# Optimization experiments

Hardware: AMD Instinct MI355X
Metric: run time of the kernel (lower is better)

Reference implementation:

```python
import jax, jax.numpy as jnp
import numpy as np

BS, T, N, E = 4, 6, 400, 3000
D = 100        # object_dim == state_dim == out_fts (forced by code)
NS = 30        # num states
NOBJ = 300     # object vocab
NET = 10       # n edge types
NSTEPS = 3     # GatedGraphConv n_steps


def setup_inputs() -> dict:
    key = jax.random.key(0)
    ks = jax.random.split(key, 16)
    def nrm(k, shape, s=0.05):
        return jax.random.normal(k, shape, jnp.float32) * s
    return dict(
        class_names=jax.random.randint(ks[0], (BS, T, N), 0, NOBJ),
        states=jax.random.uniform(ks[1], (BS, T, N, NS), jnp.float32),
        edges=jax.random.randint(ks[2], (BS, T, E, 2), 0, N),
        edge_types=jax.random.randint(ks[3], (BS, T, E), 0, NET),
        visibility=jax.random.uniform(ks[4], (BS, T, N), jnp.float32),
        mask_edges=jnp.ones((BS, T, E), jnp.float32),
        obj_emb=nrm(ks[5], (NOBJ, D)),
        state_W=nrm(ks[6], (D, NS)), state_b=jnp.zeros((D,), jnp.float32),
        c1_W=nrm(ks[7], (D, 2 * D)), c1_b=jnp.zeros((D,), jnp.float32),
        c2_W=nrm(ks[8], (D, D)), c2_b=jnp.zeros((D,), jnp.float32),
        edge_embed=nrm(ks[9], (NET, D * D)),
        g_wih=nrm(ks[10], (3 * D, D)), g_whh=nrm(ks[11], (3 * D, D)),
        g_bih=jnp.zeros((3 * D,), jnp.float32), g_bhh=jnp.zeros((3 * D,), jnp.float32),
        o_wih=nrm(ks[12], (3 * D, D)), o_whh=nrm(ks[13], (3 * D, D)),
    )


def _gru(x, h, wih, whh, bih=None, bhh=None):
    # torch.nn.GRUCell semantics
    gi = x @ wih.T
    gh = h @ whh.T
    if bih is not None:
        gi = gi + bih
        gh = gh + bhh
    ir, iz, inn = jnp.split(gi, 3, axis=-1)
    hr, hz, hn = jnp.split(gh, 3, axis=-1)
    r = jax.nn.sigmoid(ir + hr)
    z = jax.nn.sigmoid(iz + hz)
    n = jnp.tanh(inn + r * hn)
    return (1.0 - z) * n + z * h


def reference(class_names, states, edges, edge_types, visibility, mask_edges,
              obj_emb, state_W, state_b, c1_W, c1_b, c2_W, c2_b,
              edge_embed, g_wih, g_whh, g_bih, g_bhh, o_wih, o_whh):
    bs, t_len, n = class_names.shape
    # initial node representation (ClassNameStateRepresentation)
    emb = obj_emb[class_names]                       # [bs,T,N,D]
    st = states @ state_W.T + state_b                # [bs,T,N,D]
    x = jnp.concatenate([emb, st], -1)
    x = jax.nn.relu(x @ c1_W.T + c1_b) @ c2_W.T + c2_b  # [bs,T,N,D]

    off = (jnp.arange(bs) * n)[:, None]              # flatten batch into node axis
    h = jnp.zeros((bs * n, D), x.dtype)              # outer temporal GRU state
    reprs = []
    for t in range(t_len):
        h = _gru(x[:, t].reshape(bs * n, D), h, o_wih, o_whh)  # bias=False
        feat_flat = h                                 # [bs*N, D]
        src = (edges[:, t, :, 0] + off).reshape(-1)   # [bs*E]
        dst = (edges[:, t, :, 1] + off).reshape(-1)
        # per-edge DxD matrices, masked (as in original)
        W = edge_embed[edge_types[:, t].reshape(-1)].reshape(-1, D, D)
        W = W * mask_edges[:, t].reshape(-1)[:, None, None]
        # NOTE: original never updates feat_flat inside the n_steps loop,
        # so every step reads the same source features; we replicate that.
        feat_out = feat_flat
        for _ in range(NSTEPS):
            msg = jnp.einsum('eij,ej->ei', W, feat_flat[src])           # per-edge matvec
            a = jax.ops.segment_sum(msg, dst, num_segments=bs * n)     # scatter-add
            feat_out = _gru(a, feat_flat, g_wih, g_whh, g_bih, g_bhh)
        reprs.append(feat_out.reshape(bs, n, D) * visibility[:, t, :, None])
    node_reprs = jnp.stack(reprs, 1)                  # [bs,T,N,D]
    num_nodes = visibility.sum(-1) + 1e-9             # [bs,T]
    global_repr = (node_reprs * visibility[..., None]).sum(2) / num_nodes[..., None]
    return node_reprs, global_repr
```

## Files before the change

kernel.cpp:

```cpp
#include <hip/hip_runtime.h>

#define BSZ   4
#define TT    6
#define NNODE 400
#define EED   3000
#define DDIM  100
#define NSDIM 30
#define NETYP 10
#define BN    (BSZ*NNODE)
#define NROW  (BSZ*TT*NNODE)
#define NEDGE (BSZ*TT*EED)
#define KPAD  1024

#define OFF_PRE1 0
#define OFF_QT   30000
#define OFF_BQ   33000
#define OFF_BF   33104
#define OFF_WIT  33408
#define OFF_BI   63408
#define OFF_BH   63744
#define OFF_WFH  64080
#define OFF_WFL  85584
#define OFF_WOH  107088
#define OFF_WOL  128592
#define OFF_BWF  150096
#define OFF_BWPK 450096
#define OFF_WHPK 622128
#define OFF_HALL 643632
#define OFF_UB   1603632
#define OFF_CNT  6518832
#define OFF_START 6528432
#define OFF_CUR  6538036
#define OFF_SE   6547636
#define OFF_INV  6619648
#define OFF_GI   6619680

typedef __attribute__((ext_vector_type(8))) short bf16x8;
typedef __attribute__((ext_vector_type(4))) float f32x4;

__device__ __forceinline__ float sigf(float v) { return 1.0f / (1.0f + expf(-v)); }

__device__ __forceinline__ short bfc(float f) {
    union { float f; unsigned u; } v; v.f = f;
    unsigned r = v.u + 0x7fffu + ((v.u >> 16) & 1u);
    return (short)(r >> 16);
}

__device__ __forceinline__ float bf2f(short h) {
    union { unsigned u; float f; } x; x.u = ((unsigned)(unsigned short)h) << 16;
    return x.f;
}

__device__ __forceinline__ unsigned cvtpk(float lo, float hi) {
    unsigned r;
    asm("v_cvt_pk_bf16_f32 %0, %1, %2" : "=v"(r) : "v"(lo), "v"(hi));
    return r;
}

__global__ __launch_bounds__(256) void k_front(
    const float* __restrict__ obj_emb, const float* __restrict__ c1_W,
    const float* __restrict__ c1_b, const float* __restrict__ state_W,
    const float* __restrict__ state_b, const float* __restrict__ c2_W,
    const float* __restrict__ c2_b, const float* __restrict__ o_wih,
    const float* __restrict__ o_whh, const float* __restrict__ g_wih,
    const float* __restrict__ g_bih, const float* __restrict__ g_bhh,
    const float* __restrict__ vis,
    float* __restrict__ pre1, float* __restrict__ QT, float* __restrict__ bQ,
    float* __restrict__ bfold, float* __restrict__ WiT,
    float* __restrict__ bI, float* __restrict__ bH,
    ushort* __restrict__ WFH, ushort* __restrict__ WFL,
    ushort* __restrict__ WOH, ushort* __restrict__ WOL,
    float* __restrict__ inv_nv, float* __restrict__ gout, int* __restrict__ cnt) {
    int i = blockIdx.x * 256 + threadIdx.x;
    if (i < 30000) {
        int cls = i / DDIM, d1 = i % DDIM;
        float acc = 0.f;
        for (int k = 0; k < DDIM; ++k)
            acc += obj_emb[cls * DDIM + k] * c1_W[d1 * 2 * DDIM + k];
        pre1[i] = acc;
    } else if (i < 33000) {
        int j = i - 30000, s = j / DDIM, d1 = j % DDIM;
        float acc = 0.f;
        for (int d = 0; d < DDIM; ++d)
            acc += c1_W[d1 * 2 * DDIM + DDIM + d] * state_W[d * NSDIM + s];
        QT[j] = acc;
    } else if (i < 33100) {
        int d1 = i - 33000;
        float acc = c1_b[d1];
        for (int d = 0; d < DDIM; ++d)
            acc += state_b[d] * c1_W[d1 * 2 * DDIM + DDIM + d];
        bQ[d1] = acc;
    } else if (i < 33400) {
        int o = i - 33100;
        float acc = 0.f;
        for (int d = 0; d < DDIM; ++d)
            acc += o_wih[o * DDIM + d] * c2_b[d];
        bfold[o] = acc;
    } else if (i < 76408) {
        int e = i - 33400;
        int j = e & 7, frag = e >> 3;
        int l = frag & 63, ct = (frag >> 6) % 21, kt = frag / (21 * 64);
        int col = ct * 16 + (l & 15);
        int gate = col / 112, dd = col % 112;
        int k = kt * 32 + ((l >> 4) << 3) + j;
        float v = 0.f;
        if (k < DDIM && dd < DDIM) {
            int o = gate * DDIM + dd;
            for (int d = 0; d < DDIM; ++d)
                v += o_wih[o * DDIM + d] * c2_W[d * DDIM + k];
        }
        short hi = bfc(v);
        WFH[frag * 8 + j] = (ushort)hi;
        WFL[frag * 8 + j] = (ushort)bfc(v - bf2f(hi));
    } else if (i < 119416) {
        int e = i - 76408;
        int j = e & 7, frag = e >> 3;
        int l = frag & 63, ct = (frag >> 6) % 21, kt = frag / (21 * 64);
        int col = ct * 16 + (l & 15);
        int gate = col / 112, dd = col % 112;
        int k = kt * 32 + ((l >> 4) << 3) + j;
        float v = 0.f;
        if (k < DDIM && dd < DDIM)
            v = o_whh[(gate * DDIM + dd) * DDIM + k];
        short hi = bfc(v);
        WOH[frag * 8 + j] = (ushort)hi;
        WOL[frag * 8 + j] = (ushort)bfc(v - bf2f(hi));
    } else if (i < 149416) {
        int j = i - 119416, k = j / 300, o = j % 300;
        WiT[j] = g_wih[o * DDIM + k];
    } else if (i < 149752) {
        int col = i - 149416, gate = col / 112, o = col % 112;
        bI[col] = (o < DDIM) ? g_bih[gate * DDIM + o] : 0.f;
    } else if (i < 150088) {
        int col = i - 149752, gate = col / 112, o = col % 112;
        bH[col] = (o < DDIM) ? g_bhh[gate * DDIM + o] : 0.f;
    } else if (i >= 150144 && i < 151680) {
        int g = (i - 150144) >> 6;
        int lane = i & 63;
        float s = 0.f;
        for (int n = lane; n < NNODE; n += 64)
            s += vis[g * NNODE + n];
        #pragma unroll
        for (int off = 32; off > 0; off >>= 1)
            s += __shfl_down(s, off, 64);
        if (lane == 0) inv_nv[g] = 1.f / (s + 1e-9f);
    } else if (i >= 151680 && i < 154080) {
        gout[i - 151680] = 0.f;
    } else if (i >= 154080 && i < 163680) {
        cnt[i - 154080] = 0;
    }
}

__global__ __launch_bounds__(448) void k_mid(
    const float* __restrict__ edge_embed, const float* __restrict__ WiT,
    float* __restrict__ BW,
    const int* __restrict__ cls, const float* __restrict__ states,
    const float* __restrict__ pre1, const float* __restrict__ QT,
    const float* __restrict__ bQ, const float* __restrict__ bfold,
    const bf16x8* __restrict__ WFH, const bf16x8* __restrict__ WFL,
    float* __restrict__ GI,
    const int* __restrict__ edges, int* __restrict__ cnt) {
    __shared__ float st_lds[16 * NSDIM];
    __shared__ float hid_lds[16 * 112];
    __shared__ int cls_lds[16];
    int tid = threadIdx.x;
    if (blockIdx.x >= 1270) {
        int fe = (blockIdx.x - 1270) * 448 + tid;
        if (fe < NEDGE) {
            int dst = edges[fe * 2 + 1];
            int b = fe / (TT * EED), t = (fe / EED) % TT;
            atomicAdd(&cnt[t * BN + b * NNODE + dst], 1);
        }
        return;
    }
    if (blockIdx.x < 670) {
        int i = blockIdx.x * 448 + tid;
        if (i < 1000 * 300) {
            int kk = i / 300, go = i % 300;
            int g = kk / DDIM, k = kk % DDIM;
            const float* es = edge_embed + g * DDIM * DDIM + k;
            float acc = 0.f;
            for (int j = 0; j < DDIM; ++j)
                acc += es[j * DDIM] * WiT[j * 300 + go];
            BW[i] = acc;
        }
        return;
    }
    int r0 = (blockIdx.x - 670) * 16;
    for (int idx = tid; idx < 16 * NSDIM; idx += 448) st_lds[idx] = states[r0 * NSDIM + idx];
    if (tid < 16) cls_lds[tid] = cls[r0 + tid];
    __syncthreads();
    #pragma unroll
    for (int u = 0; u < 4; ++u) {
        int it = tid + u * 448;
        if (it < 1600) {
            int n = it / 100, d = it % 100;
            float acc = bQ[d] + pre1[cls_lds[n] * DDIM + d];
            for (int s = 0; s < NSDIM; ++s)
                acc += QT[s * DDIM + d] * st_lds[n * NSDIM + s];
            hid_lds[n * 112 + d] = fmaxf(acc, 0.f);
        }
    }
    __syncthreads();
    int w = tid >> 6, l = tid & 63, rit = l & 15, kgrp = l >> 4;
    f32x4 acc3[3];
    acc3[0] = acc3[1] = acc3[2] = (f32x4){0.f, 0.f, 0.f, 0.f};
    for (int kt = 0; kt < 4; ++kt) {
        bf16x8 Ahi, Alo;
        #pragma unroll
        for (int j = 0; j < 8; ++j) {
            int k = kt * 32 + kgrp * 8 + j;
            float v = (k < DDIM) ? hid_lds[rit * 112 + k] : 0.f;
            short hi = bfc(v);
            Ahi[j] = hi;
            Alo[j] = bfc(v - bf2f(hi));
        }
        #pragma unroll
        for (int p = 0; p < 3; ++p) {
            int ct = w + p * 7;
            bf16x8 Bhi = WFH[(kt * 21 + ct) * 64 + l];
            bf16x8 Blo = WFL[(kt * 21 + ct) * 64 + l];
            acc3[p] = __builtin_amdgcn_mfma_f32_16x16x32_bf16(Ahi, Bhi, acc3[p], 0, 0, 0);
            acc3[p] = __builtin_amdgcn_mfma_f32_16x16x32_bf16(Alo, Bhi, acc3[p], 0, 0, 0);
            acc3[p] = __builtin_amdgcn_mfma_f32_16x16x32_bf16(Ahi, Blo, acc3[p], 0, 0, 0);
        }
    }
    int dd = w * 16 + rit;
    if (dd < DDIM) {
        int b = r0 / (TT * NNODE), t = (r0 / NNODE) % TT, nn0 = r0 % NNODE;
        int trow0 = t * BN + b * NNODE + nn0;
        #pragma unroll
        for (int p = 0; p < 3; ++p) {
            float bias = bfold[p * DDIM + dd];
            #pragma unroll
            for (int j = 0; j < 4; ++j) {
                int row = kgrp * 4 + j;
                GI[(trow0 + row) * 336 + p * 112 + dd] = acc3[p][j] + bias;
            }
        }
    }
}

__global__ __launch_bounds__(448) void k_mid2(const float* __restrict__ GI,
    const bf16x8* __restrict__ WOH, const bf16x8* __restrict__ WOL,
    float* __restrict__ Hall,
    const float* __restrict__ BW, const float* __restrict__ g_whh,
    bf16x8* __restrict__ BWpk, bf16x8* __restrict__ WHpk,
    const int* __restrict__ cnt, int* __restrict__ start, int* __restrict__ cursor) {
    __shared__ float h_lds[16 * 112];
    int tid = threadIdx.x;
    if (blockIdx.x >= 208) {
        int c = blockIdx.x - 208;
        if (tid < 64) {
            int lane = tid;
            int carry = 0;
            for (int ch = 0; ch < 7; ++ch) {
                int idx = ch * 64 + lane;
                int orig = (idx < 400) ? cnt[c * 400 + idx] : 0;
                int v = orig;
                #pragma unroll
                for (int off = 1; off < 64; off <<= 1) {
                    int u = __shfl_up(v, off, 64);
                    if (lane >= off) v += u;
                }
                int st = c * 3000 + carry + (v - orig);
                if (idx < 400) { start[c * 400 + idx] = st; cursor[c * 400 + idx] = st; }
                carry += __shfl(v, 63, 64);
            }
            if (c == 23 && lane == 0) start[NROW] = NEDGE;
        }
        return;
    }
    if (blockIdx.x >= 100) {
        int i = (blockIdx.x - 100) * 448 + tid;
        if (i < 43008) {
            int l = i & 63, c = (i >> 6) % 21, kt = i / (21 * 64);
            int col = c * 16 + (l & 15);
            int gate = col / 112, o = col % 112;
            bf16x8 r;
            #pragma unroll
            for (int j = 0; j < 8; ++j) {
                int kk = kt * 32 + ((l >> 4) << 3) + j;
                float v = (kk < 1000 && o < DDIM) ? BW[kk * 300 + gate * DDIM + o] : 0.f;
                r[j] = bfc(v);
            }
            BWpk[i] = r;
        } else if (i < 48384) {
            int id = i - 43008;
            int l = id & 63, c = (id >> 6) % 21, kt2 = id / (21 * 64);
            int col = c * 16 + (l & 15);
            int gate = col / 112, o = col % 112;
            bf16x8 r;
            #pragma unroll
            for (int j = 0; j < 8; ++j) {
                int k = kt2 * 32 + ((l >> 4) << 3) + j;
                float v = (k < DDIM && o < DDIM) ? g_whh[(gate * DDIM + o) * DDIM + k] : 0.f;
                r[j] = bfc(v);
            }
            WHpk[id] = r;
        }
        return;
    }
    int bn0 = blockIdx.x * 16;
    for (int idx = tid; idx < 16 * 112; idx += 448) h_lds[idx] = 0.f;
    __syncthreads();
    int w = tid >> 6, l = tid & 63, rit = l & 15, kgrp = l >> 4;
    int dd = w * 16 + rit;
    for (int t = 0; t < TT; ++t) {
        float gir[4], giz[4], gin[4], hold[4];
        if (dd < DDIM) {
            #pragma unroll
            for (int j = 0; j < 4; ++j) {
                int node = kgrp * 4 + j;
                int trow = t * BN + bn0 + node;
                gir[j] = GI[trow * 336 + dd];
                giz[j] = GI[trow * 336 + 112 + dd];
                gin[j] = GI[trow * 336 + 224 + dd];
                hold[j] = h_lds[node * 112 + dd];
            }
        }
        f32x4 a0 = (f32x4){0.f, 0.f, 0.f, 0.f};
        f32x4 a1 = (f32x4){0.f, 0.f, 0.f, 0.f};
        f32x4 a2 = (f32x4){0.f, 0.f, 0.f, 0.f};
        if (t > 0) {
            for (int kt = 0; kt < 4; ++kt) {
                bf16x8 Ahi, Alo;
                #pragma unroll
                for (int j = 0; j < 8; ++j) {
                    int k = kt * 32 + kgrp * 8 + j;
                    float v = (k < DDIM) ? h_lds[rit * 112 + k] : 0.f;
                    short hi = bfc(v);
                    Ahi[j] = hi;
                    Alo[j] = bfc(v - bf2f(hi));
                }
                {
                    bf16x8 Bhi = WOH[(kt * 21 + w) * 64 + l];
                    bf16x8 Blo = WOL[(kt * 21 + w) * 64 + l];
                    a0 = __builtin_amdgcn_mfma_f32_16x16x32_bf16(Ahi, Bhi, a0, 0, 0, 0);
                    a0 = __builtin_amdgcn_mfma_f32_16x16x32_bf16(Alo, Bhi, a0, 0, 0, 0);
                    a0 = __builtin_amdgcn_mfma_f32_16x16x32_bf16(Ahi, Blo, a0, 0, 0, 0);
                }
                {
                    bf16x8 Bhi = WOH[(kt * 21 + w + 7) * 64 + l];
                    bf16x8 Blo = WOL[(kt * 21 + w + 7) * 64 + l];
                    a1 = __builtin_amdgcn_mfma_f32_16x16x32_bf16(Ahi, Bhi, a1, 0, 0, 0);
                    a1 = __builtin_amdgcn_mfma_f32_16x16x32_bf16(Alo, Bhi, a1, 0, 0, 0);
                    a1 = __builtin_amdgcn_mfma_f32_16x16x32_bf16(Ahi, Blo, a1, 0, 0, 0);
                }
                {
                    bf16x8 Bhi = WOH[(kt * 21 + w + 14) * 64 + l];
                    bf16x8 Blo = WOL[(kt * 21 + w + 14) * 64 + l];
                    a2 = __builtin_amdgcn_mfma_f32_16x16x32_bf16(Ahi, Bhi, a2, 0, 0, 0);
                    a2 = __builtin_amdgcn_mfma_f32_16x16x32_bf16(Alo, Bhi, a2, 0, 0, 0);
                    a2 = __builtin_amdgcn_mfma_f32_16x16x32_bf16(Ahi, Blo, a2, 0, 0, 0);
                }
            }
        }
        __syncthreads();
        if (dd < DDIM) {
            #pragma unroll
            for (int j = 0; j < 4; ++j) {
                int node = kgrp * 4 + j;
                int trow = t * BN + bn0 + node;
                float r = sigf(gir[j] + a0[j]);
                float z = sigf(giz[j] + a1[j]);
                float nn = tanhf(gin[j] + r * a2[j]);
                float hnew = (1.f - z) * nn + z * hold[j];
                h_lds[node * 112 + dd] = hnew;
                Hall[trow * DDIM + dd] = hnew;
            }
        }
        __syncthreads();
    }
}

__global__ __launch_bounds__(256) void k_fill(const int* __restrict__ edges,
    int* __restrict__ cursor, int* __restrict__ sortedE) {
    int fe = blockIdx.x * 256 + threadIdx.x;
    if (fe >= NEDGE) return;
    int dst = edges[fe * 2 + 1];
    int b = fe / (TT * EED), t = (fe / EED) % TT;
    int pos = atomicAdd(&cursor[t * BN + b * NNODE + dst], 1);
    sortedE[pos] = fe;
}

template<int G>
__device__ __forceinline__ void gacc(float* acc, const float* __restrict__ hs,
                                     float m, int l) {
    constexpr int k0 = 100 * G, k1 = k0 + 100;
    constexpr int J0 = k0 / 64, J1 = (k1 - 1) / 64;
    #pragma unroll
    for (int j = J0; j <= J1; ++j) {
        int k = 64 * j + l;
        if (k >= k0 && k < k1) acc[j] += m * hs[k - k0];
    }
}

__global__ __launch_bounds__(256) void k_gather(const int* __restrict__ edges,
    const int* __restrict__ etype, const float* __restrict__ emask,
    const float* __restrict__ Hall, const int* __restrict__ start,
    const int* __restrict__ sortedE, ushort* __restrict__ Ub) {
    int gid = blockIdx.x * 256 + threadIdx.x;
    int trd = gid >> 6, l = gid & 63;
    int s0 = start[trd], s1 = start[trd + 1];
    int rowbase = (trd / NNODE) * NNODE;
    float acc[16];
    #pragma unroll
    for (int j = 0; j < 16; ++j) acc[j] = 0.f;
    for (int e = s0; e < s1; ++e) {
        int fe = sortedE[e];
        float m = emask[fe];
        int src = edges[fe * 2 + 0];
        int g = etype[fe];
        const float* hs = Hall + (size_t)(rowbase + src) * DDIM;
        switch (g) {
            case 0: gacc<0>(acc, hs, m, l); break;
            case 1: gacc<1>(acc, hs, m, l); break;
            case 2: gacc<2>(acc, hs, m, l); break;
            case 3: gacc<3>(acc, hs, m, l); break;
            case 4: gacc<4>(acc, hs, m, l); break;
            case 5: gacc<5>(acc, hs, m, l); break;
            case 6: gacc<6>(acc, hs, m, l); break;
            case 7: gacc<7>(acc, hs, m, l); break;
            case 8: gacc<8>(acc, hs, m, l); break;
            case 9: gacc<9>(acc, hs, m, l); break;
        }
    }
    ushort* urow = Ub + (size_t)trd * KPAD;
    #pragma unroll
    for (int j = 0; j < 16; ++j)
        urow[64 * j + l] = (ushort)bfc(acc[j]);
}

__global__ __launch_bounds__(448) void k_fused32(const ushort* __restrict__ Ub,
    const bf16x8* __restrict__ BWpk, const bf16x8* __restrict__ WHpk,
    const float* __restrict__ bI, const float* __restrict__ bH,
    const float* __restrict__ Hall, const float* __restrict__ visv,
    const float* __restrict__ inv_nv, float* __restrict__ out,
    float* __restrict__ gout) {
    __shared__ unsigned lds[16384];
    int tid = threadIdx.x;
    int w = tid >> 6, l = tid & 63;
    int rit = l & 15, kgrp = l >> 4;
    int rbase = blockIdx.x * 32;

    for (int i = tid; i < 4096; i += 448) {
        int row = i >> 7, g16 = i & 127;
        int4 wv = *(const int4*)(Ub + (size_t)(rbase + row) * KPAD + g16 * 8);
        int wd = row * 512 + ((g16 * 4) ^ ((row & 7) << 2));
        *(int4*)&lds[wd] = wv;
    }
    __syncthreads();

    f32x4 acc[2][3];
    #pragma unroll
    for (int mt = 0; mt < 2; ++mt)
        #pragma unroll
        for (int q = 0; q < 3; ++q) acc[mt][q] = (f32x4){0.f, 0.f, 0.f, 0.f};

    for (int kt = 0; kt < 32; ++kt) {
        bf16x8 fb0 = BWpk[(kt * 21 + w) * 64 + l];
        bf16x8 fb1 = BWpk[(kt * 21 + w + 7) * 64 + l];
        bf16x8 fb2 = BWpk[(kt * 21 + w + 14) * 64 + l];
        #pragma unroll
        for (int mt = 0; mt < 2; ++mt) {
            int row = mt * 16 + rit;
            int wd = row * 512 + (((kt * 16 + kgrp * 4)) ^ ((row & 7) << 2));
            bf16x8 fa = *(bf16x8*)&lds[wd];
            acc[mt][0] = __builtin_amdgcn_mfma_f32_16x16x32_bf16(fa, fb0, acc[mt][0], 0, 0, 0);
            acc[mt][1] = __builtin_amdgcn_mfma_f32_16x16x32_bf16(fa, fb1, acc[mt][1], 0, 0, 0);
            acc[mt][2] = __builtin_amdgcn_mfma_f32_16x16x32_bf16(fa, fb2, acc[mt][2], 0, 0, 0);
        }
    }
    __syncthreads();

    for (int i = tid; i < 512; i += 448) {
        int row = i >> 4, g16 = i & 15;
        int k0 = g16 * 8;
        const float* hs = Hall + (size_t)(rbase + row) * DDIM;
        float v[8];
        #pragma unroll
        for (int jj = 0; jj < 8; ++jj)
            v[jj] = (k0 + jj < DDIM) ? hs[k0 + jj] : 0.f;
        int4 wv;
        wv.x = (int)cvtpk(v[0], v[1]);
        wv.y = (int)cvtpk(v[2], v[3]);
        wv.z = (int)cvtpk(v[4], v[5]);
        wv.w = (int)cvtpk(v[6], v[7]);
        int wd = row * 64 + ((g16 * 4) ^ ((row & 7) << 2));
        *(int4*)&lds[wd] = wv;
    }
    __syncthreads();

    f32x4 hacc[2];
    hacc[0] = (f32x4){0.f, 0.f, 0.f, 0.f};
    hacc[1] = (f32x4){0.f, 0.f, 0.f, 0.f};
    for (int kt2 = 0; kt2 < 4; ++kt2) {
        bf16x8 fb0 = WHpk[(kt2 * 21 + w) * 64 + l];
        bf16x8 fb1 = WHpk[(kt2 * 21 + w + 7) * 64 + l];
        bf16x8 fb2 = WHpk[(kt2 * 21 + w + 14) * 64 + l];
        #pragma unroll
        for (int mt = 0; mt < 2; ++mt) {
            int row = mt * 16 + rit;
            int wd = row * 64 + (((kt2 * 16 + kgrp * 4)) ^ ((row & 7) << 2));
            bf16x8 fh = *(bf16x8*)&lds[wd];
            acc[mt][0] = __builtin_amdgcn_mfma_f32_16x16x32_bf16(fh, fb0, acc[mt][0], 0, 0, 0);
            acc[mt][1] = __builtin_amdgcn_mfma_f32_16x16x32_bf16(fh, fb1, acc[mt][1], 0, 0, 0);
            hacc[mt]  = __builtin_amdgcn_mfma_f32_16x16x32_bf16(fh, fb2, hacc[mt], 0, 0, 0);
        }
    }

    int col = w * 16 + rit;
    if (col < DDIM) {
        float bIr = bI[col], bIz = bI[112 + col], bIn = bI[224 + col];
        float bHr = bH[col], bHz = bH[112 + col], bHn = bH[224 + col];
        int t = rbase / BN;
        #pragma unroll
        for (int mt = 0; mt < 2; ++mt) {
            int r2 = (rbase + mt * 16) % BN;
            int b = r2 / NNODE, n0 = r2 % NNODE;
            int bt = b * TT + t;
            int trow0 = rbase + mt * 16 + kgrp * 4;
            int brow0 = bt * NNODE + n0 + kgrp * 4;
            float gs = 0.f;
            #pragma unroll
            for (int j = 0; j < 4; ++j) {
                float r = sigf(acc[mt][0][j] + bIr + bHr);
                float z = sigf(acc[mt][1][j] + bIz + bHz);
                float ghn = hacc[mt][j] + bHn;
                float nn = tanhf(acc[mt][2][j] + bIn + r * ghn);
                float hold = Hall[(trow0 + j) * DDIM + col];
                float feat = (1.f - z) * nn + z * hold;
                int brow = brow0 + j;
                float v = visv[brow];
                float outv = feat * v;
                out[brow * DDIM + col] = outv;
                gs += outv * v;
            }
            gs += __shfl_xor(gs, 16, 64);
            gs += __shfl_xor(gs, 32, 64);
            if (kgrp == 0)
                atomicAdd(&gout[bt * DDIM + col], gs * inv_nv[bt]);
        }
    }
}

extern "C" void kernel_launch(void* const* d_in, const int* in_sizes, int n_in,
                              void* d_out, int out_size, void* d_ws, size_t ws_size,
                              hipStream_t stream) {
    const int*   class_names = (const int*)d_in[0];
    const float* states      = (const float*)d_in[1];
    const int*   edges       = (const int*)d_in[2];
    const int*   edge_types  = (const int*)d_in[3];
    const float* visibility  = (const float*)d_in[4];
    const float* mask_edges  = (const float*)d_in[5];
    const float* obj_emb     = (const float*)d_in[6];
    const float* state_W     = (const float*)d_in[7];
    const float* state_b     = (const float*)d_in[8];
    const float* c1_W        = (const float*)d_in[9];
    const float* c1_b        = (const float*)d_in[10];
    const float* c2_W        = (const float*)d_in[11];
    const float* c2_b        = (const float*)d_in[12];
    const float* edge_embed  = (const float*)d_in[13];
    const float* g_wih       = (const float*)d_in[14];
    const float* g_whh       = (const float*)d_in[15];
    const float* g_bih       = (const float*)d_in[16];
    const float* g_bhh       = (const float*)d_in[17];
    const float* o_wih       = (const float*)d_in[18];
    const float* o_whh       = (const float*)d_in[19];

    float* out = (float*)d_out;
    float* gout = out + (size_t)NROW * DDIM;
    float* ws  = (float*)d_ws;
    float*  pre1  = ws + OFF_PRE1;
    float*  QT    = ws + OFF_QT;
    float*  bQ    = ws + OFF_BQ;
    float*  bfold = ws + OFF_BF;
    float*  WiT   = ws + OFF_WIT;
    float*  bI    = ws + OFF_BI;
    float*  bH    = ws + OFF_BH;
    ushort* WFH   = (ushort*)(ws + OFF_WFH);
    ushort* WFL   = (ushort*)(ws + OFF_WFL);
    ushort* WOH   = (ushort*)(ws + OFF_WOH);
    ushort* WOL   = (ushort*)(ws + OFF_WOL);
    float*  BWf   = ws + OFF_BWF;
    bf16x8* BWpk  = (bf16x8*)(ws + OFF_BWPK);
    bf16x8* WHpk  = (bf16x8*)(ws + OFF_WHPK);
    float*  Hall  = ws + OFF_HALL;
    ushort* Ub    = (ushort*)(ws + OFF_UB);
    int*    cnt   = (int*)(ws + OFF_CNT);
    int*    start = (int*)(ws + OFF_START);
    int*    cursor= (int*)(ws + OFF_CUR);
    int*    sortedE = (int*)(ws + OFF_SE);
    float*  inv_nv= ws + OFF_INV;
    float*  GI    = ws + OFF_GI;

    k_front<<<640, 256, 0, stream>>>(obj_emb, c1_W, c1_b, state_W, state_b,
                                     c2_W, c2_b, o_wih, o_whh, g_wih, g_bih, g_bhh,
                                     visibility, pre1, QT, bQ, bfold, WiT, bI, bH,
                                     WFH, WFL, WOH, WOL, inv_nv, gout, cnt);
    k_mid<<<1431, 448, 0, stream>>>(edge_embed, WiT, BWf, class_names, states,
                                    pre1, QT, bQ, bfold,
                                    (const bf16x8*)WFH, (const bf16x8*)WFL, GI,
                                    edges, cnt);
    k_mid2<<<232, 448, 0, stream>>>(GI, (const bf16x8*)WOH, (const bf16x8*)WOL,
                                    Hall, BWf, g_whh, BWpk, WHpk,
                                    cnt, start, cursor);
    k_fill<<<(NEDGE + 255) / 256, 256, 0, stream>>>(edges, cursor, sortedE);
    k_gather<<<NROW / 4, 256, 0, stream>>>(edges, edge_types, mask_edges, Hall,
                                           start, sortedE, Ub);
    k_fused32<<<NROW / 32, 448, 0, stream>>>(Ub, BWpk, WHpk, bI, bH, Hall,
                                             visibility, inv_nv, out, gout);
}
```

Before: 114.3 us.

## Build CSR in shared memory and fuse edge gather into GRU kernel

Counting sort of edges by destination (histogram, scan, fill) now runs per graph inside 24 blocks of the front kernel using LDS atomics, replacing the global count, scan and fill passes. The separate gather kernel and its bf16 intermediate buffer go away: the fused GRU kernel gathers edge messages straight into its LDS A-tile, using float2 loads and packed bf16 conversion. This removes two launches and a large global round trip. In exchange, the gather is serialized across 7 waves per 32-row block ahead of the MFMA work, and the sort runs in only 24 blocks.

```diff
diff --git a/kernel.cpp b/kernel.cpp
--- a/kernel.cpp
+++ b/kernel.cpp
@@ -27,13 +27,10 @@
 #define OFF_BWPK 450096
 #define OFF_WHPK 622128
 #define OFF_HALL 643632
-#define OFF_UB   1603632
-#define OFF_CNT  6518832
-#define OFF_START 6528432
-#define OFF_CUR  6538036
-#define OFF_SE   6547636
-#define OFF_INV  6619648
-#define OFF_GI   6619680
+#define OFF_START 1603632
+#define OFF_SE   1613236
+#define OFF_INV  1685248
+#define OFF_GI   1685280
 
 typedef __attribute__((ext_vector_type(8))) short bf16x8;
 typedef __attribute__((ext_vector_type(4))) float f32x4;
@@ -64,14 +61,57 @@
     const float* __restrict__ c2_b, const float* __restrict__ o_wih,
     const float* __restrict__ o_whh, const float* __restrict__ g_wih,
     const float* __restrict__ g_bih, const float* __restrict__ g_bhh,
-    const float* __restrict__ vis,
+    const float* __restrict__ vis, const int* __restrict__ edges,
     float* __restrict__ pre1, float* __restrict__ QT, float* __restrict__ bQ,
     float* __restrict__ bfold, float* __restrict__ WiT,
     float* __restrict__ bI, float* __restrict__ bH,
     ushort* __restrict__ WFH, ushort* __restrict__ WFL,
     ushort* __restrict__ WOH, ushort* __restrict__ WOL,
-    float* __restrict__ inv_nv, float* __restrict__ gout, int* __restrict__ cnt) {
-    int i = blockIdx.x * 256 + threadIdx.x;
+    float* __restrict__ inv_nv, float* __restrict__ gout,
+    int* __restrict__ start, int* __restrict__ sortedE) {
+    int tid = threadIdx.x;
+    if (blockIdx.x < 24) {
+        __shared__ int hcnt[400];
+        __shared__ int hstart[400];
+        int c = blockIdx.x;
+        int t = c >> 2, b = c & 3;
+        int febase = (b * TT + t) * EED;
+        for (int i = tid; i < 400; i += 256) hcnt[i] = 0;
+        __syncthreads();
+        for (int i = tid; i < EED; i += 256)
+            atomicAdd(&hcnt[edges[(febase + i) * 2 + 1]], 1);
+        __syncthreads();
+        if (tid < 64) {
+            int lane = tid, carry = 0;
+            for (int ch = 0; ch < 7; ++ch) {
+                int idx = ch * 64 + lane;
+                int orig = (idx < 400) ? hcnt[idx] : 0;
+                int v = orig;
+                #pragma unroll
+                for (int off = 1; off < 64; off <<= 1) {
+                    int u = __shfl_up(v, off, 64);
+                    if (lane >= off) v += u;
+                }
+                if (idx < 400) hstart[idx] = carry + (v - orig);
+                carry += __shfl(v, 63, 64);
+            }
+        }
+        __syncthreads();
+        for (int i = tid; i < 400; i += 256) {
+            start[c * 400 + i] = c * EED + hstart[i];
+            hcnt[i] = hstart[i];
+        }
+        if (c == 23 && tid == 0) start[NROW] = NEDGE;
+        __syncthreads();
+        for (int i = tid; i < EED; i += 256) {
+            int fe = febase + i;
+            int dst = edges[fe * 2 + 1];
+            int pos = atomicAdd(&hcnt[dst], 1);
+            sortedE[c * EED + pos] = fe;
+        }
+        return;
+    }
+    int i = (blockIdx.x - 24) * 256 + tid;
     if (i < 30000) {
         int cls = i / DDIM, d1 = i % DDIM;
         float acc = 0.f;
@@ -146,8 +186,6 @@
         if (lane == 0) inv_nv[g] = 1.f / (s + 1e-9f);
     } else if (i >= 151680 && i < 154080) {
         gout[i - 151680] = 0.f;
-    } else if (i >= 154080 && i < 163680) {
-        cnt[i - 154080] = 0;
     }
 }
 
@@ -158,21 +196,11 @@
     const float* __restrict__ pre1, const float* __restrict__ QT,
     const float* __restrict__ bQ, const float* __restrict__ bfold,
     const bf16x8* __restrict__ WFH, const bf16x8* __restrict__ WFL,
-    float* __restrict__ GI,
-    const int* __restrict__ edges, int* __restrict__ cnt) {
+    float* __restrict__ GI) {
     __shared__ float st_lds[16 * NSDIM];
     __shared__ float hid_lds[16 * 112];
     __shared__ int cls_lds[16];
     int tid = threadIdx.x;
-    if (blockIdx.x >= 1270) {
-        int fe = (blockIdx.x - 1270) * 448 + tid;
-        if (fe < NEDGE) {
-            int dst = edges[fe * 2 + 1];
-            int b = fe / (TT * EED), t = (fe / EED) % TT;
-            atomicAdd(&cnt[t * BN + b * NNODE + dst], 1);
-        }
-        return;
-    }
     if (blockIdx.x < 670) {
         int i = blockIdx.x * 448 + tid;
         if (i < 1000 * 300) {
@@ -245,32 +273,9 @@
     const bf16x8* __restrict__ WOH, const bf16x8* __restrict__ WOL,
     float* __restrict__ Hall,
     const float* __restrict__ BW, const float* __restrict__ g_whh,
-    bf16x8* __restrict__ BWpk, bf16x8* __restrict__ WHpk,
-    const int* __restrict__ cnt, int* __restrict__ start, int* __restrict__ cursor) {
+    bf16x8* __restrict__ BWpk, bf16x8* __restrict__ WHpk) {
     __shared__ float h_lds[16 * 112];
     int tid = threadIdx.x;
-    if (blockIdx.x >= 208) {
-        int c = blockIdx.x - 208;
-        if (tid < 64) {
-            int lane = tid;
-            int carry = 0;
-            for (int ch = 0; ch < 7; ++ch) {
-                int idx = ch * 64 + lane;
-                int orig = (idx < 400) ? cnt[c * 400 + idx] : 0;
-                int v = orig;
-                #pragma unroll
-                for (int off = 1; off < 64; off <<= 1) {
-                    int u = __shfl_up(v, off, 64);
-                    if (lane >= off) v += u;
-                }
-                int st = c * 3000 + carry + (v - orig);
-                if (idx < 400) { start[c * 400 + idx] = st; cursor[c * 400 + idx] = st; }
-                carry += __shfl(v, 63, 64);
-            }
-            if (c == 23 && lane == 0) start[NROW] = NEDGE;
-        }
-        return;
-    }
     if (blockIdx.x >= 100) {
         int i = (blockIdx.x - 100) * 448 + tid;
         if (i < 43008) {
@@ -374,65 +379,26 @@
     }
 }
 
-__global__ __launch_bounds__(256) void k_fill(const int* __restrict__ edges,
-    int* __restrict__ cursor, int* __restrict__ sortedE) {
-    int fe = blockIdx.x * 256 + threadIdx.x;
-    if (fe >= NEDGE) return;
-    int dst = edges[fe * 2 + 1];
-    int b = fe / (TT * EED), t = (fe / EED) % TT;
-    int pos = atomicAdd(&cursor[t * BN + b * NNODE + dst], 1);
-    sortedE[pos] = fe;
-}
-
 template<int G>
-__device__ __forceinline__ void gacc(float* acc, const float* __restrict__ hs,
-                                     float m, int l) {
+__device__ __forceinline__ void gacc2(float* acc, const float* __restrict__ hs,
+                                      float m, int l) {
     constexpr int k0 = 100 * G, k1 = k0 + 100;
-    constexpr int J0 = k0 / 64, J1 = (k1 - 1) / 64;
+    constexpr int J0 = k0 >> 7, J1 = (k1 - 1) >> 7;
     #pragma unroll
     for (int j = J0; j <= J1; ++j) {
-        int k = 64 * j + l;
-        if (k >= k0 && k < k1) acc[j] += m * hs[k - k0];
-    }
-}
-
-__global__ __launch_bounds__(256) void k_gather(const int* __restrict__ edges,
-    const int* __restrict__ etype, const float* __restrict__ emask,
-    const float* __restrict__ Hall, const int* __restrict__ start,
-    const int* __restrict__ sortedE, ushort* __restrict__ Ub) {
-    int gid = blockIdx.x * 256 + threadIdx.x;
-    int trd = gid >> 6, l = gid & 63;
-    int s0 = start[trd], s1 = start[trd + 1];
-    int rowbase = (trd / NNODE) * NNODE;
-    float acc[16];
-    #pragma unroll
-    for (int j = 0; j < 16; ++j) acc[j] = 0.f;
-    for (int e = s0; e < s1; ++e) {
-        int fe = sortedE[e];
-        float m = emask[fe];
-        int src = edges[fe * 2 + 0];
-        int g = etype[fe];
-        const float* hs = Hall + (size_t)(rowbase + src) * DDIM;
-        switch (g) {
-            case 0: gacc<0>(acc, hs, m, l); break;
-            case 1: gacc<1>(acc, hs, m, l); break;
-            case 2: gacc<2>(acc, hs, m, l); break;
-            case 3: gacc<3>(acc, hs, m, l); break;
-            case 4: gacc<4>(acc, hs, m, l); break;
-            case 5: gacc<5>(acc, hs, m, l); break;
-            case 6: gacc<6>(acc, hs, m, l); break;
-            case 7: gacc<7>(acc, hs, m, l); break;
-            case 8: gacc<8>(acc, hs, m, l); break;
-            case 9: gacc<9>(acc, hs, m, l); break;
-        }
-    }
-    ushort* urow = Ub + (size_t)trd * KPAD;
-    #pragma unroll
-    for (int j = 0; j < 16; ++j)
-        urow[64 * j + l] = (ushort)bfc(acc[j]);
-}
-
-__global__ __launch_bounds__(448) void k_fused32(const ushort* __restrict__ Ub,
+        int s = 128 * j + 2 * l;
+        if (s >= k0 && s < k1) {
+            float2 hv = *(const float2*)(hs + (s - k0));
+            acc[2 * j]     += m * hv.x;
+            acc[2 * j + 1] += m * hv.y;
+        }
+    }
+}
+
+__global__ __launch_bounds__(448) void k_fused32(
+    const int* __restrict__ edges, const int* __restrict__ etype,
+    const float* __restrict__ emask, const int* __restrict__ start,
+    const int* __restrict__ sortedE,
     const bf16x8* __restrict__ BWpk, const bf16x8* __restrict__ WHpk,
     const float* __restrict__ bI, const float* __restrict__ bH,
     const float* __restrict__ Hall, const float* __restrict__ visv,
@@ -444,11 +410,39 @@
     int rit = l & 15, kgrp = l >> 4;
     int rbase = blockIdx.x * 32;
 
-    for (int i = tid; i < 4096; i += 448) {
-        int row = i >> 7, g16 = i & 127;
-        int4 wv = *(const int4*)(Ub + (size_t)(rbase + row) * KPAD + g16 * 8);
-        int wd = row * 512 + ((g16 * 4) ^ ((row & 7) << 2));
-        *(int4*)&lds[wd] = wv;
+    for (int r = w; r < 32; r += 7) {
+        int trd = rbase + r;
+        int s0 = start[trd], s1 = start[trd + 1];
+        int rowbase = (trd / NNODE) * NNODE;
+        float acc[16];
+        #pragma unroll
+        for (int j = 0; j < 16; ++j) acc[j] = 0.f;
+        for (int e = s0; e < s1; ++e) {
+            int fe = sortedE[e];
+            float m = emask[fe];
+            int src = edges[fe * 2 + 0];
+            int g = etype[fe];
+            const float* hs = Hall + (size_t)(rowbase + src) * DDIM;
+            switch (g) {
+                case 0: gacc2<0>(acc, hs, m, l); break;
+                case 1: gacc2<1>(acc, hs, m, l); break;
+                case 2: gacc2<2>(acc, hs, m, l); break;
+                case 3: gacc2<3>(acc, hs, m, l); break;
+                case 4: gacc2<4>(acc, hs, m, l); break;
+                case 5: gacc2<5>(acc, hs, m, l); break;
+                case 6: gacc2<6>(acc, hs, m, l); break;
+                case 7: gacc2<7>(acc, hs, m, l); break;
+                case 8: gacc2<8>(acc, hs, m, l); break;
+                case 9: gacc2<9>(acc, hs, m, l); break;
+            }
+        }
+        #pragma unroll
+        for (int j = 0; j < 8; ++j) {
+            unsigned word = cvtpk(acc[2 * j], acc[2 * j + 1]);
+            int g16 = 16 * j + (l >> 2);
+            int wd = r * 512 + ((g16 * 4) ^ ((r & 7) << 2)) + (l & 3);
+            lds[wd] = word;
+        }
     }
     __syncthreads();
 
@@ -587,28 +581,22 @@
     bf16x8* BWpk  = (bf16x8*)(ws + OFF_BWPK);
     bf16x8* WHpk  = (bf16x8*)(ws + OFF_WHPK);
     float*  Hall  = ws + OFF_HALL;
-    ushort* Ub    = (ushort*)(ws + OFF_UB);
-    int*    cnt   = (int*)(ws + OFF_CNT);
     int*    start = (int*)(ws + OFF_START);
-    int*    cursor= (int*)(ws + OFF_CUR);
     int*    sortedE = (int*)(ws + OFF_SE);
     float*  inv_nv= ws + OFF_INV;
     float*  GI    = ws + OFF_GI;
 
-    k_front<<<640, 256, 0, stream>>>(obj_emb, c1_W, c1_b, state_W, state_b,
+    k_front<<<626, 256, 0, stream>>>(obj_emb, c1_W, c1_b, state_W, state_b,
                                      c2_W, c2_b, o_wih, o_whh, g_wih, g_bih, g_bhh,
-                                     visibility, pre1, QT, bQ, bfold, WiT, bI, bH,
-                                     WFH, WFL, WOH, WOL, inv_nv, gout, cnt);
-    k_mid<<<1431, 448, 0, stream>>>(edge_embed, WiT, BWf, class_names, states,
+                                     visibility, edges, pre1, QT, bQ, bfold, WiT,
+                                     bI, bH, WFH, WFL, WOH, WOL, inv_nv, gout,
+                                     start, sortedE);
+    k_mid<<<1270, 448, 0, stream>>>(edge_embed, WiT, BWf, class_names, states,
                                     pre1, QT, bQ, bfold,
-                                    (const bf16x8*)WFH, (const bf16x8*)WFL, GI,
-                                    edges, cnt);
-    k_mid2<<<232, 448, 0, stream>>>(GI, (const bf16x8*)WOH, (const bf16x8*)WOL,
-                                    Hall, BWf, g_whh, BWpk, WHpk,
-                                    cnt, start, cursor);
-    k_fill<<<(NEDGE + 255) / 256, 256, 0, stream>>>(edges, cursor, sortedE);
-    k_gather<<<NROW / 4, 256, 0, stream>>>(edges, edge_types, mask_edges, Hall,
-                                           start, sortedE, Ub);
-    k_fused32<<<NROW / 32, 448, 0, stream>>>(Ub, BWpk, WHpk, bI, bH, Hall,
-                                             visibility, inv_nv, out, gout);
-}
+                                    (const bf16x8*)WFH, (const bf16x8*)WFL, GI);
+    k_mid2<<<208, 448, 0, stream>>>(GI, (const bf16x8*)WOH, (const bf16x8*)WOL,
+                                    Hall, BWf, g_whh, BWpk, WHpk);
+    k_fused32<<<NROW / 32, 448, 0, stream>>>(edges, edge_types, mask_edges,
+                                             start, sortedE, BWpk, WHpk, bI, bH,
+                                             Hall, visibility, inv_nv, out, gout);
+}
```

Result: slower. 128.0 us (+12.0%).
